# Kernel optimization log

Measured on AMD Instinct MI355X. Metric: run time of the kernel, lower is better.

Reference implementation:

```python
import jax, jax.numpy as jnp
import numpy as np

N, F, B = 4096, 2048, 2048


def setup_inputs() -> dict:
    key = jax.random.key(0)
    ks = jax.random.split(key, 11)
    s_h = 1.0 / np.sqrt(F).astype(np.float32)
    s_x = 1.0 / np.sqrt(B).astype(np.float32)
    inp = {
        "behavior": jax.random.normal(ks[0], (N, B), jnp.float32),
        "h0": jax.random.normal(ks[1], (N, F), jnp.float32),
        "c0": jax.random.normal(ks[2], (N, F), jnp.float32),
        "Wi_h": jax.random.normal(ks[3], (F, F), jnp.float32) * s_h,
        "Wi_x": jax.random.normal(ks[4], (B, F), jnp.float32) * s_x,
        "bi": jnp.zeros((F,), jnp.float32),
        "Wf_h": jax.random.normal(ks[5], (F, F), jnp.float32) * s_h,
        "Wf_x": jax.random.normal(ks[6], (B, F), jnp.float32) * s_x,
        "bf": jnp.zeros((F,), jnp.float32),
        "Wg_h": jax.random.normal(ks[7], (F, F), jnp.float32) * s_h,
        "Wg_x": jax.random.normal(ks[8], (B, F), jnp.float32) * s_x,
        "bg": jnp.zeros((F,), jnp.float32),
        "Wo_h": jax.random.normal(ks[9], (F, F), jnp.float32) * s_h,
        "Wo_x": jax.random.normal(ks[10], (B, F), jnp.float32) * s_x,
        "bo": jnp.zeros((F,), jnp.float32),
    }
    return inp


def reference(behavior, h0, c0, Wi_h, Wi_x, bi, Wf_h, Wf_x, bf,
              Wg_h, Wg_x, bg, Wo_h, Wo_x, bo):
    # Single-step LSTM cell: each gate is a two-input linear proj (h, behavior)
    def proj(Wh, Wx, b):
        return h0 @ Wh + behavior @ Wx + b  # [N, F]

    i = jax.nn.sigmoid(proj(Wi_h, Wi_x, bi))
    f = jax.nn.sigmoid(proj(Wf_h, Wf_x, bf))
    g = jnp.tanh(proj(Wg_h, Wg_x, bg))
    o = jax.nn.sigmoid(proj(Wo_h, Wo_x, bo))
    c = f * c0 + i * g
    h = o * jnp.tanh(c)
    return h
```

## Files before the change

### kernel.cpp

```cpp
#include <hip/hip_runtime.h>
#include <stdint.h>

#define N_ROWS 4096
#define F_DIM  2048
#define B_DIM  2048
#define K_DIM  4096

typedef __attribute__((ext_vector_type(8))) __bf16 bf16x8;
typedef __attribute__((ext_vector_type(4))) float  f32x4;
typedef unsigned short u16;

__device__ __forceinline__ u16 f2bf(float x) {
  unsigned int u = __float_as_uint(x);
  u += 0x7fffu + ((u >> 16) & 1u);
  return (u16)(u >> 16);
}

__device__ __forceinline__ void async_copy16(const void* g, void* l) {
  __builtin_amdgcn_global_load_lds(
      (const __attribute__((address_space(1))) void*)g,
      (__attribute__((address_space(3))) void*)l, 16, 0, 0);
}

__device__ __forceinline__ float sigmoid_f(float x) {
  return 1.0f / (1.0f + __expf(-x));
}
__device__ __forceinline__ float tanh_f(float x) {
  float e2 = __expf(2.0f * x);
  return 1.0f - 2.0f / (e2 + 1.0f);
}

__global__ __launch_bounds__(256) void pack_x_kernel(
    const float* __restrict__ h0, const float* __restrict__ behavior,
    u16* __restrict__ Xc)
{
  int tid = blockIdx.x * 256 + threadIdx.x;
  int row = tid >> 9;
  int k0  = (tid & 511) * 8;
  const float* src = (k0 < F_DIM) ? (h0 + (size_t)row * F_DIM + k0)
                                  : (behavior + (size_t)row * B_DIM + (k0 - F_DIM));
  const float4* s4 = (const float4*)src;
  float4 a = s4[0], b = s4[1];
  uint4 o;
  o.x = (unsigned)f2bf(a.x) | ((unsigned)f2bf(a.y) << 16);
  o.y = (unsigned)f2bf(a.z) | ((unsigned)f2bf(a.w) << 16);
  o.z = (unsigned)f2bf(b.x) | ((unsigned)f2bf(b.y) << 16);
  o.w = (unsigned)f2bf(b.z) | ((unsigned)f2bf(b.w) << 16);
  *(uint4*)(Xc + (size_t)tid * 8) = o;
}

__global__ __launch_bounds__(256) void pack_w_kernel(
    const float* __restrict__ wi_h, const float* __restrict__ wi_x,
    const float* __restrict__ wf_h, const float* __restrict__ wf_x,
    const float* __restrict__ wg_h, const float* __restrict__ wg_x,
    const float* __restrict__ wo_h, const float* __restrict__ wo_x,
    u16* __restrict__ WT)
{
  __shared__ float tile[32][33];
  int g = blockIdx.z;
  const float* Wh = (g == 0) ? wi_h : (g == 1) ? wf_h : (g == 2) ? wg_h : wo_h;
  const float* Wx = (g == 0) ? wi_x : (g == 1) ? wf_x : (g == 2) ? wg_x : wo_x;
  int fb = blockIdx.x * 32;
  int kb = blockIdx.y * 32;
  int tx = threadIdx.x & 31;
  int ty = threadIdx.x >> 5;
#pragma unroll
  for (int r = 0; r < 4; ++r) {
    int k = kb + ty + r * 8;
    int f = fb + tx;
    float v = (k < F_DIM) ? Wh[(size_t)k * F_DIM + f]
                          : Wx[(size_t)(k - F_DIM) * F_DIM + f];
    tile[ty + r * 8][tx] = v;
  }
  __syncthreads();
#pragma unroll
  for (int r = 0; r < 4; ++r) {
    int fl = ty + r * 8;
    int kl = tx;
    WT[((size_t)g * F_DIM + fb + fl) * K_DIM + kb + kl] = f2bf(tile[kl][fl]);
  }
}

__global__ __launch_bounds__(256) void lstm_gemm_kernel(
    const u16* __restrict__ Xc, const u16* __restrict__ WT,
    const float* __restrict__ c0,
    const float* __restrict__ bi, const float* __restrict__ bff,
    const float* __restrict__ bg, const float* __restrict__ bo,
    float* __restrict__ out)
{
  __shared__ u16 As[128 * 64];
  __shared__ u16 Bs[4 * 32 * 64];

  const int tid  = threadIdx.x;
  const int lane = tid & 63;
  const int wv   = tid >> 6;
  const int bn   = blockIdx.x;
  const int bm   = blockIdx.y;

  const u16* agp[4];
  const u16* bgp[4];
#pragma unroll
  for (int j = 0; j < 4; ++j) {
    int c = j * 256 + tid;
    int r = c >> 3, s = c & 7, o = s ^ (r & 7);
    agp[j] = Xc + (size_t)(bm * 128 + r) * K_DIM + o * 8;
  }
#pragma unroll
  for (int j = 0; j < 4; ++j) {
    int r = tid >> 3, s = tid & 7, o = s ^ (r & 7);
    bgp[j] = WT + ((size_t)j * F_DIM + bn * 32 + r) * K_DIM + o * 8;
  }
  const unsigned ubase = (unsigned)(tid & ~63) * 16u;

  f32x4 acc[4][2][2];
  const f32x4 zero = {0.f, 0.f, 0.f, 0.f};
#pragma unroll
  for (int g = 0; g < 4; ++g)
#pragma unroll
    for (int rh = 0; rh < 2; ++rh)
#pragma unroll
      for (int cf = 0; cf < 2; ++cf) acc[g][rh][cf] = zero;

  const int q = lane >> 4, ln15 = lane & 15;

  for (int kt = 0; kt < 64; ++kt) {
#pragma unroll
    for (int j = 0; j < 4; ++j)
      async_copy16(agp[j], (char*)As + j * 4096 + ubase);
#pragma unroll
    for (int j = 0; j < 4; ++j)
      async_copy16(bgp[j], (char*)Bs + j * 4096 + ubase);
#pragma unroll
    for (int j = 0; j < 4; ++j) { agp[j] += 64; bgp[j] += 64; }
    __syncthreads();

#pragma unroll
    for (int c = 0; c < 2; ++c) {
      bf16x8 af[2];
#pragma unroll
      for (int rh = 0; rh < 2; ++rh) {
        int m = wv * 32 + rh * 16 + ln15;
        int o = c * 4 + q;
        int s = o ^ (m & 7);
        af[rh] = *(const bf16x8*)(As + m * 64 + s * 8);
      }
      bf16x8 bfr[4][2];
#pragma unroll
      for (int g = 0; g < 4; ++g)
#pragma unroll
        for (int cf = 0; cf < 2; ++cf) {
          int n = cf * 16 + ln15;
          int o = c * 4 + q;
          int s = o ^ (n & 7);
          bfr[g][cf] = *(const bf16x8*)(Bs + g * 2048 + n * 64 + s * 8);
        }
#pragma unroll
      for (int g = 0; g < 4; ++g)
#pragma unroll
        for (int rh = 0; rh < 2; ++rh)
#pragma unroll
          for (int cf = 0; cf < 2; ++cf)
            acc[g][rh][cf] = __builtin_amdgcn_mfma_f32_16x16x32_bf16(
                af[rh], bfr[g][cf], acc[g][rh][cf], 0, 0, 0);
    }
    __syncthreads();
  }

#pragma unroll
  for (int cf = 0; cf < 2; ++cf) {
    int col = bn * 32 + cf * 16 + ln15;
    float b0 = bi[col], b1 = bff[col], b2 = bg[col], b3 = bo[col];
#pragma unroll
    for (int rh = 0; rh < 2; ++rh) {
      int row0 = bm * 128 + wv * 32 + rh * 16 + q * 4;
#pragma unroll
      for (int r = 0; r < 4; ++r) {
        size_t idx = (size_t)(row0 + r) * F_DIM + col;
        float pi = acc[0][rh][cf][r] + b0;
        float pf = acc[1][rh][cf][r] + b1;
        float pg = acc[2][rh][cf][r] + b2;
        float po = acc[3][rh][cf][r] + b3;
        float iv = sigmoid_f(pi);
        float fv = sigmoid_f(pf);
        float gv = tanh_f(pg);
        float ov = sigmoid_f(po);
        float cv = fv * c0[idx] + iv * gv;
        out[idx] = ov * tanh_f(cv);
      }
    }
  }
}

extern "C" void kernel_launch(void* const* d_in, const int* in_sizes, int n_in,
                              void* d_out, int out_size, void* d_ws, size_t ws_size,
                              hipStream_t stream) {
  const float* behavior = (const float*)d_in[0];
  const float* h0       = (const float*)d_in[1];
  const float* c0       = (const float*)d_in[2];
  const float* Wi_h     = (const float*)d_in[3];
  const float* Wi_x     = (const float*)d_in[4];
  const float* bi       = (const float*)d_in[5];
  const float* Wf_h     = (const float*)d_in[6];
  const float* Wf_x     = (const float*)d_in[7];
  const float* bf       = (const float*)d_in[8];
  const float* Wg_h     = (const float*)d_in[9];
  const float* Wg_x     = (const float*)d_in[10];
  const float* bg       = (const float*)d_in[11];
  const float* Wo_h     = (const float*)d_in[12];
  const float* Wo_x     = (const float*)d_in[13];
  const float* bo       = (const float*)d_in[14];
  float* out = (float*)d_out;

  u16* Xc = (u16*)d_ws;
  u16* WT = Xc + (size_t)N_ROWS * K_DIM;

  pack_x_kernel<<<dim3(N_ROWS * (K_DIM / 8) / 256), 256, 0, stream>>>(h0, behavior, Xc);
  pack_w_kernel<<<dim3(F_DIM / 32, K_DIM / 32, 4), 256, 0, stream>>>(
      Wi_h, Wi_x, Wf_h, Wf_x, Wg_h, Wg_x, Wo_h, Wo_x, WT);
  lstm_gemm_kernel<<<dim3(F_DIM / 32, N_ROWS / 128), 256, 0, stream>>>(
      Xc, WT, c0, bi, bf, bg, bo, out);
}
```

Measured before the change: 556.9 us.

## Shrink GEMM M-tile to 64, swap grid order, vectorize weight transpose pack

The fused LSTM GEMM now uses a 64-row by 32-column (x4 gates) block tile instead of 128x32, with one A fragment per wave, and the grid is reordered so consecutive blocks walk along M sharing the same weight column slice. The weight pack kernel moves to 64x64 tiles with float4 loads and 16-byte bf16 stores. The intent is more blocks for occupancy, better L2 reuse of weight tiles, and a cheaper pack step. In exchange each block does half the MFMAs per loaded B tile, which raises LDS and global traffic per flop.

```diff
diff --git a/kernel.cpp b/kernel.cpp
--- a/kernel.cpp
+++ b/kernel.cpp
@@ -56,28 +56,40 @@
     const float* __restrict__ wo_h, const float* __restrict__ wo_x,
     u16* __restrict__ WT)
 {
-  __shared__ float tile[32][33];
+  __shared__ float tileT[64 * 65];
   int g = blockIdx.z;
   const float* Wh = (g == 0) ? wi_h : (g == 1) ? wf_h : (g == 2) ? wg_h : wo_h;
   const float* Wx = (g == 0) ? wi_x : (g == 1) ? wf_x : (g == 2) ? wg_x : wo_x;
-  int fb = blockIdx.x * 32;
-  int kb = blockIdx.y * 32;
-  int tx = threadIdx.x & 31;
-  int ty = threadIdx.x >> 5;
+  int fb = blockIdx.x * 64;
+  int kb = blockIdx.y * 64;
+  const float* W = (kb < F_DIM) ? Wh : Wx;
+  int kofs = (kb < F_DIM) ? kb : (kb - F_DIM);
+
+  int t  = threadIdx.x;
+  int c4 = t & 15;
+  int kl = t >> 4;
 #pragma unroll
   for (int r = 0; r < 4; ++r) {
-    int k = kb + ty + r * 8;
-    int f = fb + tx;
-    float v = (k < F_DIM) ? Wh[(size_t)k * F_DIM + f]
-                          : Wx[(size_t)(k - F_DIM) * F_DIM + f];
-    tile[ty + r * 8][tx] = v;
+    int k_l = kl + r * 16;
+    float4 v = *(const float4*)(W + (size_t)(kofs + k_l) * F_DIM + fb + c4 * 4);
+    tileT[(c4 * 4 + 0) * 65 + k_l] = v.x;
+    tileT[(c4 * 4 + 1) * 65 + k_l] = v.y;
+    tileT[(c4 * 4 + 2) * 65 + k_l] = v.z;
+    tileT[(c4 * 4 + 3) * 65 + k_l] = v.w;
   }
   __syncthreads();
 #pragma unroll
-  for (int r = 0; r < 4; ++r) {
-    int fl = ty + r * 8;
-    int kl = tx;
-    WT[((size_t)g * F_DIM + fb + fl) * K_DIM + kb + kl] = f2bf(tile[kl][fl]);
+  for (int it = 0; it < 2; ++it) {
+    int idx = it * 256 + t;
+    int f_l = idx >> 3;
+    int k8  = (idx & 7) * 8;
+    const float* s = tileT + f_l * 65 + k8;
+    uint4 o;
+    o.x = (unsigned)f2bf(s[0]) | ((unsigned)f2bf(s[1]) << 16);
+    o.y = (unsigned)f2bf(s[2]) | ((unsigned)f2bf(s[3]) << 16);
+    o.z = (unsigned)f2bf(s[4]) | ((unsigned)f2bf(s[5]) << 16);
+    o.w = (unsigned)f2bf(s[6]) | ((unsigned)f2bf(s[7]) << 16);
+    *(uint4*)(WT + ((size_t)g * F_DIM + fb + f_l) * K_DIM + kb + k8) = o;
   }
 }
 
@@ -88,22 +100,22 @@
     const float* __restrict__ bg, const float* __restrict__ bo,
     float* __restrict__ out)
 {
-  __shared__ u16 As[128 * 64];
+  __shared__ u16 As[64 * 64];
   __shared__ u16 Bs[4 * 32 * 64];
 
   const int tid  = threadIdx.x;
   const int lane = tid & 63;
   const int wv   = tid >> 6;
-  const int bn   = blockIdx.x;
-  const int bm   = blockIdx.y;
-
-  const u16* agp[4];
+  const int bm   = blockIdx.x;
+  const int bn   = blockIdx.y;
+
+  const u16* agp[2];
   const u16* bgp[4];
 #pragma unroll
-  for (int j = 0; j < 4; ++j) {
+  for (int j = 0; j < 2; ++j) {
     int c = j * 256 + tid;
     int r = c >> 3, s = c & 7, o = s ^ (r & 7);
-    agp[j] = Xc + (size_t)(bm * 128 + r) * K_DIM + o * 8;
+    agp[j] = Xc + (size_t)(bm * 64 + r) * K_DIM + o * 8;
   }
 #pragma unroll
   for (int j = 0; j < 4; ++j) {
@@ -112,37 +124,36 @@
   }
   const unsigned ubase = (unsigned)(tid & ~63) * 16u;
 
-  f32x4 acc[4][2][2];
+  f32x4 acc[4][2];
   const f32x4 zero = {0.f, 0.f, 0.f, 0.f};
 #pragma unroll
   for (int g = 0; g < 4; ++g)
 #pragma unroll
-    for (int rh = 0; rh < 2; ++rh)
-#pragma unroll
-      for (int cf = 0; cf < 2; ++cf) acc[g][rh][cf] = zero;
+    for (int cf = 0; cf < 2; ++cf) acc[g][cf] = zero;
 
   const int q = lane >> 4, ln15 = lane & 15;
 
   for (int kt = 0; kt < 64; ++kt) {
 #pragma unroll
-    for (int j = 0; j < 4; ++j)
+    for (int j = 0; j < 2; ++j)
       async_copy16(agp[j], (char*)As + j * 4096 + ubase);
 #pragma unroll
     for (int j = 0; j < 4; ++j)
       async_copy16(bgp[j], (char*)Bs + j * 4096 + ubase);
 #pragma unroll
-    for (int j = 0; j < 4; ++j) { agp[j] += 64; bgp[j] += 64; }
+    for (int j = 0; j < 2; ++j) agp[j] += 64;
+#pragma unroll
+    for (int j = 0; j < 4; ++j) bgp[j] += 64;
     __syncthreads();
 
 #pragma unroll
     for (int c = 0; c < 2; ++c) {
-      bf16x8 af[2];
-#pragma unroll
-      for (int rh = 0; rh < 2; ++rh) {
-        int m = wv * 32 + rh * 16 + ln15;
+      bf16x8 af;
+      {
+        int m = wv * 16 + ln15;
         int o = c * 4 + q;
         int s = o ^ (m & 7);
-        af[rh] = *(const bf16x8*)(As + m * 64 + s * 8);
+        af = *(const bf16x8*)(As + m * 64 + s * 8);
       }
       bf16x8 bfr[4][2];
 #pragma unroll
@@ -157,11 +168,9 @@
 #pragma unroll
       for (int g = 0; g < 4; ++g)
 #pragma unroll
-        for (int rh = 0; rh < 2; ++rh)
-#pragma unroll
-          for (int cf = 0; cf < 2; ++cf)
-            acc[g][rh][cf] = __builtin_amdgcn_mfma_f32_16x16x32_bf16(
-                af[rh], bfr[g][cf], acc[g][rh][cf], 0, 0, 0);
+        for (int cf = 0; cf < 2; ++cf)
+          acc[g][cf] = __builtin_amdgcn_mfma_f32_16x16x32_bf16(
+              af, bfr[g][cf], acc[g][cf], 0, 0, 0);
     }
     __syncthreads();
   }
@@ -170,23 +179,20 @@
   for (int cf = 0; cf < 2; ++cf) {
     int col = bn * 32 + cf * 16 + ln15;
     float b0 = bi[col], b1 = bff[col], b2 = bg[col], b3 = bo[col];
-#pragma unroll
-    for (int rh = 0; rh < 2; ++rh) {
-      int row0 = bm * 128 + wv * 32 + rh * 16 + q * 4;
-#pragma unroll
-      for (int r = 0; r < 4; ++r) {
-        size_t idx = (size_t)(row0 + r) * F_DIM + col;
-        float pi = acc[0][rh][cf][r] + b0;
-        float pf = acc[1][rh][cf][r] + b1;
-        float pg = acc[2][rh][cf][r] + b2;
-        float po = acc[3][rh][cf][r] + b3;
-        float iv = sigmoid_f(pi);
-        float fv = sigmoid_f(pf);
-        float gv = tanh_f(pg);
-        float ov = sigmoid_f(po);
-        float cv = fv * c0[idx] + iv * gv;
-        out[idx] = ov * tanh_f(cv);
-      }
+    int row0 = bm * 64 + wv * 16 + q * 4;
+#pragma unroll
+    for (int r = 0; r < 4; ++r) {
+      size_t idx = (size_t)(row0 + r) * F_DIM + col;
+      float pi = acc[0][cf][r] + b0;
+      float pf = acc[1][cf][r] + b1;
+      float pg = acc[2][cf][r] + b2;
+      float po = acc[3][cf][r] + b3;
+      float iv = sigmoid_f(pi);
+      float fv = sigmoid_f(pf);
+      float gv = tanh_f(pg);
+      float ov = sigmoid_f(po);
+      float cv = fv * c0[idx] + iv * gv;
+      out[idx] = ov * tanh_f(cv);
     }
   }
 }
@@ -215,8 +221,8 @@
   u16* WT = Xc + (size_t)N_ROWS * K_DIM;
 
   pack_x_kernel<<<dim3(N_ROWS * (K_DIM / 8) / 256), 256, 0, stream>>>(h0, behavior, Xc);
-  pack_w_kernel<<<dim3(F_DIM / 32, K_DIM / 32, 4), 256, 0, stream>>>(
+  pack_w_kernel<<<dim3(F_DIM / 64, K_DIM / 64, 4), 256, 0, stream>>>(
       Wi_h, Wi_x, Wf_h, Wf_x, Wg_h, Wg_x, Wo_h, Wo_x, WT);
-  lstm_gemm_kernel<<<dim3(F_DIM / 32, N_ROWS / 128), 256, 0, stream>>>(
+  lstm_gemm_kernel<<<dim3(N_ROWS / 64, F_DIM / 32), 256, 0, stream>>>(
       Xc, WT, c0, bi, bf, bg, bo, out);
 }
```

After: 572.3 us. 1.03x slower.
